# Performance work log

Measured on AMD Instinct MI355X. Metric: run time of the kernel, lower is better.

The kernel has to match this reference:

```python
import jax, jax.numpy as jnp
import numpy as np

B, S, F, H = 2, 2048, 2048, 16
DH = F // H  # head_dim = 128
ROPE_BASE = 10000.0


def apply_rope(x, offset):
    # x: [B, S, H, Dh]; rotate-half RoPE per head with positions offset..offset+S-1
    d = x.shape[-1]
    pos = jnp.arange(x.shape[1], dtype=jnp.float32) + offset          # [S]
    inv_freq = 1.0 / (ROPE_BASE ** (jnp.arange(0, d, 2, dtype=jnp.float32) / d))  # [Dh/2]
    ang = pos[:, None] * inv_freq[None, :]                             # [S, Dh/2]
    cos = jnp.cos(ang)[None, :, None, :].astype(x.dtype)               # [1,S,1,Dh/2]
    sin = jnp.sin(ang)[None, :, None, :].astype(x.dtype)
    x1, x2 = x[..., : d // 2], x[..., d // 2 :]
    return jnp.concatenate([x1 * cos - x2 * sin, x1 * sin + x2 * cos], axis=-1)


def setup_inputs() -> dict:
    key = jax.random.key(0)
    k0, k1, k2, k3 = jax.random.split(key, 4)
    lecun = (1.0 / F) ** 0.5
    in_q = jax.random.normal(k0, (B, S, F), dtype=jnp.float32)
    Wq = jax.random.normal(k1, (F, H, DH), dtype=jnp.float32) * lecun
    Wk = jax.random.normal(k2, (F, H, DH), dtype=jnp.float32) * lecun
    Wv = jax.random.normal(k3, (F, H, DH), dtype=jnp.float32) * lecun
    bq = jnp.zeros((H, DH), dtype=jnp.float32)
    bk = jnp.zeros((H, DH), dtype=jnp.float32)
    bv = jnp.zeros((H, DH), dtype=jnp.float32)
    mask = jnp.tril(jnp.ones((S, S), dtype=bool))[None, None, :, :]  # causal [1,1,S,S]
    return {"in_q": in_q, "Wq": Wq, "bq": bq, "Wk": Wk, "bk": bk,
            "Wv": Wv, "bv": bv, "mask": mask, "offset": 0}


def reference(in_q, Wq, bq, Wk, bk, Wv, bv, mask, offset):
    # QKV projections: LinearGeneral [B,S,F] x [F,H,Dh] -> [B,S,H,Dh]
    q = jnp.einsum("bsf,fhd->bshd", in_q, Wq) + bq
    k = jnp.einsum("bsf,fhd->bshd", in_q, Wk) + bk
    v = jnp.einsum("bsf,fhd->bshd", in_q, Wv) + bv
    # RoPE on q and k (merge/split-head reshape in original is a no-op on values)
    q = apply_rope(q, offset)
    k = apply_rope(k, offset)
    # dot-product attention
    scale = 1.0 / jnp.sqrt(jnp.asarray(DH, dtype=q.dtype))
    scores = jnp.einsum("bqhd,bkhd->bhqk", q, k) * scale   # [B,H,Sq,Skv]
    scores = jnp.where(mask, scores, jnp.finfo(scores.dtype).min)
    weights = jax.nn.softmax(scores, axis=-1)
    out = jnp.einsum("bhqk,bkhd->bqhd", weights, v)        # [B,S,H,Dh]
    return out.reshape(out.shape[0], out.shape[1], H * DH)  # merge heads
```

## Files before the change

### kernel.cpp

```cpp
#include <hip/hip_runtime.h>
#include <hip/hip_bf16.h>
#include <stdint.h>

#define NB 2
#define NS 2048
#define NFE 2048
#define NH 16
#define NDH 128

#define QSCALE (0.08838834764831845f * 1.4426950408889634f)

typedef __attribute__((ext_vector_type(4))) float f32x4;
typedef __attribute__((ext_vector_type(8))) __bf16 bf16x8;

__device__ __forceinline__ uint16_t f2bf(float f) {
  uint32_t u = __builtin_bit_cast(uint32_t, f);
  return (uint16_t)((u + 0x7fffu + ((u >> 16) & 1u)) >> 16);
}

__device__ __forceinline__ void gload_lds16(const void* g, void* l) {
  __builtin_amdgcn_global_load_lds((const __attribute__((address_space(1))) void*)g,
                                   (__attribute__((address_space(3))) void*)l,
                                   16, 0, 0);
}

#define MFMA16(a, b, c) __builtin_amdgcn_mfma_f32_16x16x32_bf16(a, b, c, 0, 0, 0)

__global__ void k_convert(const float* __restrict__ x, uint16_t* __restrict__ y) {
  int i = (blockIdx.x * 256 + threadIdx.x) * 4;
  float4 v = *(const float4*)(x + i);
  ushort4 o;
  o.x = f2bf(v.x); o.y = f2bf(v.y); o.z = f2bf(v.z); o.w = f2bf(v.w);
  *(ushort4*)(y + i) = o;
}

__global__ void k_wt(const float* __restrict__ Wq, const float* __restrict__ Wk,
                     const float* __restrict__ Wv, uint16_t* __restrict__ Wt) {
  int which = blockIdx.z;
  const float* Wsrc = (which == 0) ? Wq : ((which == 1) ? Wk : Wv);
  int k0 = blockIdx.x * 64, n0 = blockIdx.y * 64;
  __shared__ uint16_t tile[64][65];
  int t = threadIdx.x;
#pragma unroll
  for (int it = 0; it < 4; ++it) {
    int vec = t + it * 256;
    int r = vec >> 4, c4 = vec & 15;
    float4 v = *(const float4*)&Wsrc[(size_t)(k0 + r) * NFE + n0 + c4 * 4];
    tile[r][c4 * 4 + 0] = f2bf(v.x);
    tile[r][c4 * 4 + 1] = f2bf(v.y);
    tile[r][c4 * 4 + 2] = f2bf(v.z);
    tile[r][c4 * 4 + 3] = f2bf(v.w);
  }
  __syncthreads();
#pragma unroll
  for (int it = 0; it < 4; ++it) {
    int vec = t + it * 256;
    int r = vec >> 4, c4 = vec & 15;
    ushort4 o;
    o.x = tile[c4 * 4 + 0][r];
    o.y = tile[c4 * 4 + 1][r];
    o.z = tile[c4 * 4 + 2][r];
    o.w = tile[c4 * 4 + 3][r];
    *(ushort4*)&Wt[(size_t)which * NFE * NFE + (size_t)(n0 + r) * NFE + k0 + c4 * 4] = o;
  }
}

__global__ void k_rope_tab(float* __restrict__ cosT, float* __restrict__ sinT,
                           const int* __restrict__ offp) {
  int tid = blockIdx.x * 256 + threadIdx.x;
  int s = tid >> 6, i = tid & 63;
  float off = (float)offp[0];
  float inv = expf(-((float)i / 64.0f) * logf(10000.0f));
  float ang = ((float)s + off) * inv;
  cosT[tid] = cosf(ang);
  sinT[tid] = sinf(ang);
}

__global__ __launch_bounds__(256, 2) void k_gemm_qkv(
    const uint16_t* __restrict__ A, const uint16_t* __restrict__ Wt,
    const float* __restrict__ bq, const float* __restrict__ bk, const float* __restrict__ bv,
    const float* __restrict__ cosT, const float* __restrict__ sinT,
    uint16_t* __restrict__ qws, uint16_t* __restrict__ kws, uint16_t* __restrict__ vws) {
  __shared__ alignas(16) uint16_t Asm[128 * 64];
  __shared__ alignas(16) uint16_t Bsm[128 * 64];
  int mt = blockIdx.x;
  int nt = blockIdx.y;
  int which = nt >> 4, h = nt & 15;
  const uint16_t* Bsrc = Wt + (size_t)which * NFE * NFE + (size_t)h * NDH * NFE;
  const uint16_t* Arow = A + (size_t)mt * 128 * NFE;
  int t = threadIdx.x, w = t >> 6, l = t & 63;
  int g = l >> 4, c = l & 15;

  f32x4 acc[2][8];
#pragma unroll
  for (int m = 0; m < 2; ++m)
#pragma unroll
    for (int n = 0; n < 8; ++n) acc[m][n] = (f32x4){0.f, 0.f, 0.f, 0.f};

  for (int kt = 0; kt < NFE / 64; ++kt) {
    int k0 = kt * 64;
#pragma unroll
    for (int cc = 0; cc < 4; ++cc) {
      int flat = cc * 256 + t;
      int row = flat >> 3, sub = flat & 7;
      int scol = ((sub ^ (row & 7)) << 3) + k0;
      gload_lds16(&Arow[(size_t)row * NFE + scol], (char*)Asm + flat * 16);
    }
#pragma unroll
    for (int cc = 0; cc < 4; ++cc) {
      int flat = cc * 256 + t;
      int row = flat >> 3, sub = flat & 7;
      int scol = ((sub ^ (row & 7)) << 3) + k0;
      gload_lds16(&Bsrc[(size_t)row * NFE + scol], (char*)Bsm + flat * 16);
    }
    __syncthreads();
#pragma unroll
    for (int ks = 0; ks < 2; ++ks) {
      bf16x8 af[2];
#pragma unroll
      for (int m = 0; m < 2; ++m) {
        int row = w * 32 + m * 16 + c;
        int kb = ((ks * 32 + g * 8) * 2) ^ ((row & 7) << 4);
        af[m] = *(const bf16x8*)((const char*)Asm + row * 128 + kb);
      }
#pragma unroll
      for (int nf = 0; nf < 8; ++nf) {
        int row = nf * 16 + c;
        int kb = ((ks * 32 + g * 8) * 2) ^ ((row & 7) << 4);
        bf16x8 bfr = *(const bf16x8*)((const char*)Bsm + row * 128 + kb);
        acc[0][nf] = MFMA16(af[0], bfr, acc[0][nf]);
        acc[1][nf] = MFMA16(af[1], bfr, acc[1][nf]);
      }
    }
    __syncthreads();
  }

  const float* bias = (which == 0) ? bq : ((which == 1) ? bk : bv);
  uint16_t* outp = (which == 0) ? qws : ((which == 1) ? kws : vws);
  float scl = (which == 0) ? QSCALE : 1.0f;
  int mbase = mt * 128 + w * 32;
  if (which < 2) {
#pragma unroll
    for (int m = 0; m < 2; ++m)
#pragma unroll
      for (int nf = 0; nf < 4; ++nf) {
        int i = nf * 16 + c;
        float b1 = bias[h * NDH + i], b2 = bias[h * NDH + 64 + i];
#pragma unroll
        for (int j = 0; j < 4; ++j) {
          int r = mbase + m * 16 + g * 4 + j;
          int bb = r >> 11, s = r & (NS - 1);
          float cs = cosT[(s << 6) + i], sn = sinT[(s << 6) + i];
          float x1 = acc[m][nf][j] + b1;
          float x2 = acc[m][nf + 4][j] + b2;
          uint16_t* op = outp + ((size_t)(bb * NH + h) * NS + s) * NDH;
          op[i] = f2bf((x1 * cs - x2 * sn) * scl);
          op[64 + i] = f2bf((x1 * sn + x2 * cs) * scl);
        }
      }
  } else {
#pragma unroll
    for (int m = 0; m < 2; ++m)
#pragma unroll
      for (int nf = 0; nf < 8; ++nf) {
        int d = nf * 16 + c;
        float bv_ = bias[h * NDH + d];
#pragma unroll
        for (int j = 0; j < 4; ++j) {
          int r = mbase + m * 16 + g * 4 + j;
          int bb = r >> 11, s = r & (NS - 1);
          outp[((size_t)(bb * NH + h) * NS + s) * NDH + d] = f2bf(acc[m][nf][j] + bv_);
        }
      }
  }
}

__global__ void k_vt(const uint16_t* __restrict__ v, uint16_t* __restrict__ vt) {
  int bh = blockIdx.z;
  int s0 = blockIdx.x * 64, d0 = blockIdx.y * 64;
  __shared__ uint16_t tile[64][65];
  int t = threadIdx.x;
#pragma unroll
  for (int it = 0; it < 4; ++it) {
    int vec = t + it * 256;
    int r = vec >> 4, c4 = vec & 15;
    ushort4 x = *(const ushort4*)&v[((size_t)bh * NS + s0 + r) * NDH + d0 + c4 * 4];
    tile[r][c4 * 4 + 0] = x.x;
    tile[r][c4 * 4 + 1] = x.y;
    tile[r][c4 * 4 + 2] = x.z;
    tile[r][c4 * 4 + 3] = x.w;
  }
  __syncthreads();
#pragma unroll
  for (int it = 0; it < 4; ++it) {
    int vec = t + it * 256;
    int r = vec >> 4, c4 = vec & 15;
    ushort4 o;
    o.x = tile[c4 * 4 + 0][r];
    o.y = tile[c4 * 4 + 1][r];
    o.z = tile[c4 * 4 + 2][r];
    o.w = tile[c4 * 4 + 3][r];
    *(ushort4*)&vt[((size_t)bh * NDH + d0 + r) * NS + s0 + c4 * 4] = o;
  }
}

__global__ __launch_bounds__(256, 4) void k_attn(
    const uint16_t* __restrict__ qws, const uint16_t* __restrict__ kws,
    const uint16_t* __restrict__ vtws, float* __restrict__ out) {
  __shared__ alignas(16) uint16_t Ksm[64 * 128];
  __shared__ alignas(16) uint16_t Vsm[128 * 64];
  __shared__ alignas(16) uint16_t Psm[4][16 * 64];

  int bh = blockIdx.x;
  int t = threadIdx.x, w = t >> 6, l = t & 63;
  int g = l >> 4, c = l & 15;
  int bb = bh >> 4, h = bh & 15;

  const uint16_t* Qp = qws + (size_t)bh * NS * NDH;
  const uint16_t* Kp = kws + (size_t)bh * NS * NDH;
  const uint16_t* Vp = vtws + (size_t)bh * NDH * NS;

  for (int pass = 0; pass < 2; ++pass) {
    int y64 = pass ? (31 - blockIdx.y) : blockIdx.y;
    int q0 = y64 * 64;
    int r = q0 + w * 16 + c;

    bf16x8 qf[4];
#pragma unroll
    for (int kk = 0; kk < 4; ++kk)
      qf[kk] = *(const bf16x8*)&Qp[(size_t)r * NDH + kk * 32 + g * 8];

    f32x4 acc_o[8];
    float mreg = -1e30f, lreg = 0.f;
#pragma unroll
    for (int n = 0; n < 8; ++n) acc_o[n] = (f32x4){0.f, 0.f, 0.f, 0.f};

    int nkt = y64 + 1;
    for (int kt = 0; kt < nkt; ++kt) {
#pragma unroll
      for (int cc = 0; cc < 4; ++cc) {
        int flat = cc * 256 + t;
        int row = flat >> 4, sub = flat & 15;
        int scol = ((sub ^ (row & 7)) << 3);
        gload_lds16(&Kp[(size_t)(kt * 64 + row) * NDH + scol], (char*)Ksm + flat * 16);
      }
#pragma unroll
      for (int cc = 0; cc < 4; ++cc) {
        int flat = cc * 256 + t;
        int row = flat >> 3, sub = flat & 7;
        int scol = ((sub ^ (row & 7)) << 3);
        gload_lds16(&Vp[(size_t)row * NS + kt * 64 + scol], (char*)Vsm + flat * 16);
      }
      __syncthreads();

      f32x4 sacc[4];
#pragma unroll
      for (int nf = 0; nf < 4; ++nf) sacc[nf] = (f32x4){0.f, 0.f, 0.f, 0.f};
#pragma unroll
      for (int kk = 0; kk < 4; ++kk) {
#pragma unroll
        for (int nf = 0; nf < 4; ++nf) {
          int row = nf * 16 + c;
          int kb = ((kk * 32 + g * 8) * 2) ^ ((row & 7) << 4);
          bf16x8 kfr = *(const bf16x8*)((const char*)Ksm + row * 256 + kb);
          sacc[nf] = MFMA16(kfr, qf[kk], sacc[nf]);
        }
      }

      if (kt == y64) {
#pragma unroll
        for (int nf = 0; nf < 4; ++nf)
#pragma unroll
          for (int j = 0; j < 4; ++j) {
            int kv = kt * 64 + nf * 16 + g * 4 + j;
            if (kv > r) sacc[nf][j] = -1e30f;
          }
      }

      float mx = -1e30f;
#pragma unroll
      for (int nf = 0; nf < 4; ++nf)
        mx = fmaxf(mx, fmaxf(fmaxf(sacc[nf][0], sacc[nf][1]),
                             fmaxf(sacc[nf][2], sacc[nf][3])));
      mx = fmaxf(mx, __shfl_xor(mx, 16));
      mx = fmaxf(mx, __shfl_xor(mx, 32));

      float mnew = mreg;
      if (!__all(mx <= mreg + 8.0f)) {
        mnew = fmaxf(mreg, mx);
        float alpha = exp2f(mreg - mnew);
        mreg = mnew;
        lreg *= alpha;
#pragma unroll
        for (int j = 0; j < 4; ++j) {
          float aj = __shfl(alpha, (l & 48) + g * 4 + j);
#pragma unroll
          for (int nf = 0; nf < 8; ++nf) acc_o[nf][j] *= aj;
        }
      }

      float rs = 0.f;
#pragma unroll
      for (int nf = 0; nf < 4; ++nf)
#pragma unroll
        for (int j = 0; j < 4; ++j) {
          float p = exp2f(sacc[nf][j] - mnew);
          sacc[nf][j] = p;
          rs += p;
        }
      rs += __shfl_xor(rs, 16);
      rs += __shfl_xor(rs, 32);
      lreg += rs;

#pragma unroll
      for (int nf = 0; nf < 4; ++nf) {
        uint32_t pk0 = (uint32_t)f2bf(sacc[nf][0]) | ((uint32_t)f2bf(sacc[nf][1]) << 16);
        uint32_t pk1 = (uint32_t)f2bf(sacc[nf][2]) | ((uint32_t)f2bf(sacc[nf][3]) << 16);
        int colb = (nf * 16 + g * 4) * 2;
        char* base = (char*)Psm[w] + c * 128;
        *(uint32_t*)(base + (colb ^ ((c & 7) << 4))) = pk0;
        *(uint32_t*)(base + ((colb + 4) ^ ((c & 7) << 4))) = pk1;
      }

#pragma unroll
      for (int kk2 = 0; kk2 < 2; ++kk2) {
        int prow = c;
        int pkb = ((kk2 * 32 + g * 8) * 2) ^ ((prow & 7) << 4);
        bf16x8 pf = *(const bf16x8*)((const char*)Psm[w] + prow * 128 + pkb);
#pragma unroll
        for (int nf = 0; nf < 8; ++nf) {
          int row = nf * 16 + c;
          int kb = ((kk2 * 32 + g * 8) * 2) ^ ((row & 7) << 4);
          bf16x8 vf = *(const bf16x8*)((const char*)Vsm + row * 128 + kb);
          acc_o[nf] = MFMA16(pf, vf, acc_o[nf]);
        }
      }
      __syncthreads();
    }

#pragma unroll
    for (int j = 0; j < 4; ++j) {
      float lj = __shfl(lreg, (l & 48) + g * 4 + j);
      float inv = 1.0f / lj;
      int s = q0 + w * 16 + g * 4 + j;
      float* op = out + ((size_t)(bb * NS + s)) * NFE + h * NDH;
#pragma unroll
      for (int nf = 0; nf < 8; ++nf) op[nf * 16 + c] = acc_o[nf][j] * inv;
    }
  }
}

extern "C" void kernel_launch(void* const* d_in, const int* in_sizes, int n_in,
                              void* d_out, int out_size, void* d_ws, size_t ws_size,
                              hipStream_t stream) {
  const float* in_q = (const float*)d_in[0];
  const float* Wq = (const float*)d_in[1];
  const float* bq = (const float*)d_in[2];
  const float* Wk = (const float*)d_in[3];
  const float* bk = (const float*)d_in[4];
  const float* Wv = (const float*)d_in[5];
  const float* bv = (const float*)d_in[6];
  const int* offp = (const int*)d_in[8];
  float* out = (float*)d_out;

  char* ws = (char*)d_ws;
  const size_t SZ_AQ = (size_t)4096 * 2048 * 2;
  const size_t SZ_WT = (size_t)3 * 2048 * 2048 * 2;
  const size_t SZ_TAB = (size_t)2048 * 64 * 4;
  const size_t SZ_QKV = (size_t)32 * 2048 * 128 * 2;
  uint16_t* Aq = (uint16_t*)(ws);
  uint16_t* Wt = (uint16_t*)(ws + SZ_AQ);
  float* cosT = (float*)(ws + SZ_AQ + SZ_WT);
  float* sinT = (float*)(ws + SZ_AQ + SZ_WT + SZ_TAB);
  uint16_t* qws = (uint16_t*)(ws + SZ_AQ + SZ_WT + 2 * SZ_TAB);
  uint16_t* kws = (uint16_t*)(ws + SZ_AQ + SZ_WT + 2 * SZ_TAB + SZ_QKV);
  uint16_t* vws = (uint16_t*)(ws + SZ_AQ + SZ_WT + 2 * SZ_TAB + 2 * SZ_QKV);
  uint16_t* vtws = (uint16_t*)(ws + SZ_AQ + SZ_WT + 2 * SZ_TAB + 3 * SZ_QKV);

  k_convert<<<8192, 256, 0, stream>>>(in_q, Aq);
  k_wt<<<dim3(32, 32, 3), 256, 0, stream>>>(Wq, Wk, Wv, Wt);
  k_rope_tab<<<512, 256, 0, stream>>>(cosT, sinT, offp);
  k_gemm_qkv<<<dim3(32, 48), 256, 0, stream>>>(Aq, Wt, bq, bk, bv, cosT, sinT, qws, kws, vws);
  k_vt<<<dim3(32, 2, 32), 256, 0, stream>>>(vws, vtws);
  k_attn<<<dim3(32, 16), 256, 0, stream>>>(qws, kws, vtws, out);
}
```

Measured before the change: 210.2 us.

## Double-buffer attention K/V loads, swizzle GEMM grid, fuse rope table into convert

The attention kernel now double-buffers K and V tiles in LDS, prefetching the next KV tile while the current one is computed, with one barrier at the end of each iteration. The QKV GEMM uses a 1D grid with an XCD-aware block swizzle and a higher occupancy hint, and the RoPE table generation is folded into the convert kernel to save a launch. Double buffering doubles LDS use in attention (about 66KB per block), which may reduce the occupancy allowed by the launch bounds.

```diff
diff --git a/kernel.cpp b/kernel.cpp
--- a/kernel.cpp
+++ b/kernel.cpp
@@ -26,12 +26,25 @@
 
 #define MFMA16(a, b, c) __builtin_amdgcn_mfma_f32_16x16x32_bf16(a, b, c, 0, 0, 0)
 
-__global__ void k_convert(const float* __restrict__ x, uint16_t* __restrict__ y) {
-  int i = (blockIdx.x * 256 + threadIdx.x) * 4;
-  float4 v = *(const float4*)(x + i);
-  ushort4 o;
-  o.x = f2bf(v.x); o.y = f2bf(v.y); o.z = f2bf(v.z); o.w = f2bf(v.w);
-  *(ushort4*)(y + i) = o;
+__global__ void k_convert(const float* __restrict__ x, uint16_t* __restrict__ y,
+                          float* __restrict__ cosT, float* __restrict__ sinT,
+                          const int* __restrict__ offp) {
+  int b = blockIdx.x;
+  if (b < 8192) {
+    int i = (b * 256 + threadIdx.x) * 4;
+    float4 v = *(const float4*)(x + i);
+    ushort4 o;
+    o.x = f2bf(v.x); o.y = f2bf(v.y); o.z = f2bf(v.z); o.w = f2bf(v.w);
+    *(ushort4*)(y + i) = o;
+  } else {
+    int tid = (b - 8192) * 256 + threadIdx.x;
+    int s = tid >> 6, i = tid & 63;
+    float off = (float)offp[0];
+    float inv = expf(-((float)i / 64.0f) * logf(10000.0f));
+    float ang = ((float)s + off) * inv;
+    cosT[tid] = cosf(ang);
+    sinT[tid] = sinf(ang);
+  }
 }
 
 __global__ void k_wt(const float* __restrict__ Wq, const float* __restrict__ Wk,
@@ -65,26 +78,16 @@
   }
 }
 
-__global__ void k_rope_tab(float* __restrict__ cosT, float* __restrict__ sinT,
-                           const int* __restrict__ offp) {
-  int tid = blockIdx.x * 256 + threadIdx.x;
-  int s = tid >> 6, i = tid & 63;
-  float off = (float)offp[0];
-  float inv = expf(-((float)i / 64.0f) * logf(10000.0f));
-  float ang = ((float)s + off) * inv;
-  cosT[tid] = cosf(ang);
-  sinT[tid] = sinf(ang);
-}
-
-__global__ __launch_bounds__(256, 2) void k_gemm_qkv(
+__global__ __launch_bounds__(256, 4) void k_gemm_qkv(
     const uint16_t* __restrict__ A, const uint16_t* __restrict__ Wt,
     const float* __restrict__ bq, const float* __restrict__ bk, const float* __restrict__ bv,
     const float* __restrict__ cosT, const float* __restrict__ sinT,
     uint16_t* __restrict__ qws, uint16_t* __restrict__ kws, uint16_t* __restrict__ vws) {
   __shared__ alignas(16) uint16_t Asm[128 * 64];
   __shared__ alignas(16) uint16_t Bsm[128 * 64];
-  int mt = blockIdx.x;
-  int nt = blockIdx.y;
+  int bid = blockIdx.x;
+  int swzb = (bid & 7) * 192 + (bid >> 3);
+  int mt = swzb & 31, nt = swzb >> 5;
   int which = nt >> 4, h = nt & 15;
   const uint16_t* Bsrc = Wt + (size_t)which * NFE * NFE + (size_t)h * NDH * NFE;
   const uint16_t* Arow = A + (size_t)mt * 128 * NFE;
@@ -207,8 +210,8 @@
 __global__ __launch_bounds__(256, 4) void k_attn(
     const uint16_t* __restrict__ qws, const uint16_t* __restrict__ kws,
     const uint16_t* __restrict__ vtws, float* __restrict__ out) {
-  __shared__ alignas(16) uint16_t Ksm[64 * 128];
-  __shared__ alignas(16) uint16_t Vsm[128 * 64];
+  __shared__ alignas(16) uint16_t Ksm[2][64 * 128];
+  __shared__ alignas(16) uint16_t Vsm[2][128 * 64];
   __shared__ alignas(16) uint16_t Psm[4][16 * 64];
 
   int bh = blockIdx.x;
@@ -220,6 +223,24 @@
   const uint16_t* Kp = kws + (size_t)bh * NS * NDH;
   const uint16_t* Vp = vtws + (size_t)bh * NDH * NS;
 
+#define STAGE(bb_, kt_)                                                            \
+  do {                                                                             \
+    _Pragma("unroll") for (int cc = 0; cc < 4; ++cc) {                             \
+      int flat = cc * 256 + t;                                                     \
+      int row = flat >> 4, sub = flat & 15;                                        \
+      int scol = ((sub ^ (row & 7)) << 3);                                         \
+      gload_lds16(&Kp[(size_t)((kt_) * 64 + row) * NDH + scol],                    \
+                  (char*)Ksm[bb_] + flat * 16);                                    \
+    }                                                                              \
+    _Pragma("unroll") for (int cc = 0; cc < 4; ++cc) {                             \
+      int flat = cc * 256 + t;                                                     \
+      int row = flat >> 3, sub = flat & 7;                                         \
+      int scol = ((sub ^ (row & 7)) << 3);                                         \
+      gload_lds16(&Vp[(size_t)row * NS + (kt_) * 64 + scol],                       \
+                  (char*)Vsm[bb_] + flat * 16);                                    \
+    }                                                                              \
+  } while (0)
+
   for (int pass = 0; pass < 2; ++pass) {
     int y64 = pass ? (31 - blockIdx.y) : blockIdx.y;
     int q0 = y64 * 64;
@@ -236,22 +257,12 @@
     for (int n = 0; n < 8; ++n) acc_o[n] = (f32x4){0.f, 0.f, 0.f, 0.f};
 
     int nkt = y64 + 1;
+    STAGE(0, 0);
+    __syncthreads();
+
     for (int kt = 0; kt < nkt; ++kt) {
-#pragma unroll
-      for (int cc = 0; cc < 4; ++cc) {
-        int flat = cc * 256 + t;
-        int row = flat >> 4, sub = flat & 15;
-        int scol = ((sub ^ (row & 7)) << 3);
-        gload_lds16(&Kp[(size_t)(kt * 64 + row) * NDH + scol], (char*)Ksm + flat * 16);
-      }
-#pragma unroll
-      for (int cc = 0; cc < 4; ++cc) {
-        int flat = cc * 256 + t;
-        int row = flat >> 3, sub = flat & 7;
-        int scol = ((sub ^ (row & 7)) << 3);
-        gload_lds16(&Vp[(size_t)row * NS + kt * 64 + scol], (char*)Vsm + flat * 16);
-      }
-      __syncthreads();
+      int cur = kt & 1;
+      if (kt + 1 < nkt) STAGE(cur ^ 1, kt + 1);
 
       f32x4 sacc[4];
 #pragma unroll
@@ -262,7 +273,7 @@
         for (int nf = 0; nf < 4; ++nf) {
           int row = nf * 16 + c;
           int kb = ((kk * 32 + g * 8) * 2) ^ ((row & 7) << 4);
-          bf16x8 kfr = *(const bf16x8*)((const char*)Ksm + row * 256 + kb);
+          bf16x8 kfr = *(const bf16x8*)((const char*)Ksm[cur] + row * 256 + kb);
           sacc[nf] = MFMA16(kfr, qf[kk], sacc[nf]);
         }
       }
@@ -331,7 +342,7 @@
         for (int nf = 0; nf < 8; ++nf) {
           int row = nf * 16 + c;
           int kb = ((kk2 * 32 + g * 8) * 2) ^ ((row & 7) << 4);
-          bf16x8 vf = *(const bf16x8*)((const char*)Vsm + row * 128 + kb);
+          bf16x8 vf = *(const bf16x8*)((const char*)Vsm[cur] + row * 128 + kb);
           acc_o[nf] = MFMA16(pf, vf, acc_o[nf]);
         }
       }
@@ -348,6 +359,7 @@
       for (int nf = 0; nf < 8; ++nf) op[nf * 16 + c] = acc_o[nf][j] * inv;
     }
   }
+#undef STAGE
 }
 
 extern "C" void kernel_launch(void* const* d_in, const int* in_sizes, int n_in,
@@ -377,10 +389,9 @@
   uint16_t* vws = (uint16_t*)(ws + SZ_AQ + SZ_WT + 2 * SZ_TAB + 2 * SZ_QKV);
   uint16_t* vtws = (uint16_t*)(ws + SZ_AQ + SZ_WT + 2 * SZ_TAB + 3 * SZ_QKV);
 
-  k_convert<<<8192, 256, 0, stream>>>(in_q, Aq);
+  k_convert<<<8704, 256, 0, stream>>>(in_q, Aq, cosT, sinT, offp);
   k_wt<<<dim3(32, 32, 3), 256, 0, stream>>>(Wq, Wk, Wv, Wt);
-  k_rope_tab<<<512, 256, 0, stream>>>(cosT, sinT, offp);
-  k_gemm_qkv<<<dim3(32, 48), 256, 0, stream>>>(Aq, Wt, bq, bk, bv, cosT, sinT, qws, kws, vws);
+  k_gemm_qkv<<<1536, 256, 0, stream>>>(Aq, Wt, bq, bk, bv, cosT, sinT, qws, kws, vws);
   k_vt<<<dim3(32, 2, 32), 256, 0, stream>>>(vws, vtws);
   k_attn<<<dim3(32, 16), 256, 0, stream>>>(qws, kws, vtws, out);
 }
```

Measured after the change: 209.1 us. No clear change (-0.5%).
